# Kernel optimization log

Measured on AMD Instinct MI355X. Metric: run time of the kernel, lower is better.

The kernel has to match this reference:

```python
import jax, jax.numpy as jnp
import numpy as np

N = 5000
NFEAT = 512
NHID = 64
NHEADS = 8
NCLASS = 40
ALPHA = 0.2  # leaky relu slope
NEG_INF = -9e15


def setup_inputs() -> dict:
    key = jax.random.key(0)
    ks = jax.random.split(key, 12)
    x = jax.random.normal(ks[0], (N, NFEAT), dtype=jnp.float32)
    # binary adjacency, ~32 avg degree, with self loops
    adj = (jax.random.uniform(ks[1], (N, N)) < (32.0 / N)).astype(jnp.float32)
    adj = jnp.maximum(adj, jnp.eye(N, dtype=jnp.float32))
    s = 1.0 / np.sqrt(NFEAT)
    W_h = jax.random.uniform(ks[2], (NHEADS, NFEAT, NHID), minval=-s, maxval=s, dtype=jnp.float32)
    a_h = jax.random.uniform(ks[3], (NHEADS, 2 * NHID), minval=-s, maxval=s, dtype=jnp.float32)
    s2 = 1.0 / np.sqrt(NHID * NHEADS)
    W_o = jax.random.uniform(ks[4], (NHID * NHEADS, NHID), minval=-s2, maxval=s2, dtype=jnp.float32)
    a_o = jax.random.uniform(ks[5], (2 * NHID,), minval=-s2, maxval=s2, dtype=jnp.float32)
    s3 = 1.0 / np.sqrt(NHID)
    fc1_w = jax.random.uniform(ks[6], (NHID, 200), minval=-s3, maxval=s3, dtype=jnp.float32)
    fc1_b = jax.random.uniform(ks[7], (200,), minval=-s3, maxval=s3, dtype=jnp.float32)
    s4 = 1.0 / np.sqrt(200)
    fc2_w = jax.random.uniform(ks[8], (200, NCLASS), minval=-s4, maxval=s4, dtype=jnp.float32)
    fc2_b = jax.random.uniform(ks[9], (NCLASS,), minval=-s4, maxval=s4, dtype=jnp.float32)
    return {"x": x, "adj": adj, "W_h": W_h, "a_h": a_h, "W_o": W_o, "a_o": a_o,
            "fc1_w": fc1_w, "fc1_b": fc1_b, "fc2_w": fc2_w, "fc2_b": fc2_b}


def _masked_attention(e, adj):
    # e: [..., N, N]; mask where adj == 0, then row softmax
    e = jnp.where(adj > 0, e, NEG_INF)
    return jax.nn.softmax(e, axis=-1)


def reference(x, adj, W_h, a_h, W_o, a_o, fc1_w, fc1_b, fc2_w, fc2_b):
    # ---- multi-head GAT layer (concat=True), eval mode (dropout off) ----
    Wh = jnp.einsum('nf,hfo->hno', x, W_h)                 # [H, N, nhid]
    f1 = jnp.einsum('hno,ho->hn', Wh, a_h[:, :NHID])       # [H, N]
    f2 = jnp.einsum('hno,ho->hn', Wh, a_h[:, NHID:])       # [H, N]
    e = jax.nn.leaky_relu(f1[:, :, None] + f2[:, None, :], ALPHA)  # [H, N, N]
    att = _masked_attention(e, adj[None, :, :])
    h = jnp.einsum('hnm,hmo->hno', att, Wh)                # [H, N, nhid]
    h1 = jax.nn.elu(h).transpose(1, 0, 2).reshape(N, NHEADS * NHID)  # concat heads

    # ---- output GAT layer (concat=False) ----
    Wh2 = h1 @ W_o                                         # [N, nhid]
    g1 = Wh2 @ a_o[:NHID]                                  # [N]
    g2 = Wh2 @ a_o[NHID:]                                  # [N]
    e2 = jax.nn.leaky_relu(g1[:, None] + g2[None, :], ALPHA)
    att2 = _masked_attention(e2, adj)
    h2 = att2 @ Wh2                                        # [N, nhid]

    # ---- MLP head ----
    h3 = jax.nn.elu(h2 @ fc1_w + fc1_b)
    return h3 @ fc2_w + fc2_b                              # [N, nclass]
```

## Files before the change

### kernel.cpp

```cpp
#include <hip/hip_runtime.h>

typedef unsigned short u16;
typedef unsigned int u32;
typedef unsigned long long u64;
typedef __bf16 bf16_t;
typedef __bf16 bf16x8 __attribute__((ext_vector_type(8)));
typedef float f32x4 __attribute__((ext_vector_type(4)));
typedef u32 u32x4 __attribute__((ext_vector_type(4)));

#define NN 5000
#define NF 512
#define NH 64
#define HEADS 8
#define NCLS 40
#define CAP 128
#define LRELU 0.2f

#define CVT_BIG 320
#define CVT_GRID (CVT_BIG + 8)

__device__ __forceinline__ bool adj_is_bf16(const void* adj) {
    return ((*(const u32*)adj) & 0xFFFFu) != 0u;
}
__device__ __forceinline__ u16 rne_bf16(float f) {
    u32 u = __float_as_uint(f);
    u += 0x7FFFu + ((u >> 16) & 1u);
    return (u16)(u >> 16);
}
__device__ __forceinline__ float up_bf16(u16 h) {
    return __uint_as_float((u32)h << 16);
}
__device__ __forceinline__ u32x4 ntload4(const void* p, int idx) {
    return __builtin_nontemporal_load(((const u32x4*)p) + idx);
}

__global__ __launch_bounds__(256) void cvt(const void* __restrict__ x, const void* __restrict__ W_h,
                                           const void* __restrict__ adj,
                                           const void* a_h, const void* W_o, const void* a_o,
                                           const void* f1w, const void* f1b,
                                           const void* f2w, const void* f2b,
                                           u16* __restrict__ xc, u16* __restrict__ whc,
                                           float* a_hc, float* W_oc, float* a_oc,
                                           float* f1wc, float* f1bc, float* f2wc, float* f2bc) {
    const bool isb = adj_is_bf16(adj);
    const int b = blockIdx.x;
    if (b < CVT_BIG) {
        const int X4 = NN * NF / 4;
        const int T4 = X4 + HEADS * NF * NH / 4;
        for (int i = b * 256 + threadIdx.x; i < T4; i += CVT_BIG * 256) {
            const void* src; u16* dst; int off;
            if (i < X4) { src = x; dst = xc; off = i; }
            else        { src = W_h; dst = whc; off = i - X4; }
            ushort4 o;
            if (isb) {
                o = ((const ushort4*)src)[off];
            } else {
                u32x4 vv = ntload4(src, off);
                o.x = rne_bf16(__uint_as_float(vv[0])); o.y = rne_bf16(__uint_as_float(vv[1]));
                o.z = rne_bf16(__uint_as_float(vv[2])); o.w = rne_bf16(__uint_as_float(vv[3]));
            }
            ((ushort4*)dst)[off] = o;
        }
    } else {
        const int s0 = HEADS * 2 * NH, s1 = HEADS * NH * NH, s2 = 2 * NH,
                  s3 = NH * 200, s4 = 200, s5 = 200 * NCLS, s6 = NCLS;
        const int total = s0 + s1 + s2 + s3 + s4 + s5 + s6;
        for (int i = (b - CVT_BIG) * 256 + threadIdx.x; i < total; i += 8 * 256) {
            const void* src; float* dst; int off = i;
            if (off < s0) { src = a_h; dst = a_hc; }
            else if ((off -= s0) < s1) { src = W_o;  dst = W_oc; }
            else if ((off -= s1) < s2) { src = a_o;  dst = a_oc; }
            else if ((off -= s2) < s3) { src = f1w;  dst = f1wc; }
            else if ((off -= s3) < s4) { src = f1b;  dst = f1bc; }
            else if ((off -= s4) < s5) { src = f2w;  dst = f2wc; }
            else { off -= s5;           src = f2b;  dst = f2bc; }
            dst[off] = isb ? up_bf16(((const u16*)src)[off]) : ((const float*)src)[off];
        }
    }
}

__global__ __launch_bounds__(256) void gemm1_f(const bf16_t* __restrict__ x,
                                               const bf16_t* __restrict__ W_h,
                                               const float* __restrict__ a_h,
                                               float* __restrict__ Wh,
                                               float* __restrict__ f1,
                                               float* __restrict__ f2) {
    const int lane = threadIdx.x & 63;
    const int wid  = threadIdx.x >> 6;
    const int rg = blockIdx.x;
    const int h  = blockIdx.y;
    const int quad = lane >> 4;
    const int lr   = lane & 15;
    const int kq   = quad * 8;
    const int nCol = wid * 16 + lr;
    const bf16_t* Bh = W_h + (size_t)h * NF * NH;
    __shared__ float f1s[4][64], f2s[4][64];

    bf16x8 bfrag[16];
    #pragma unroll
    for (int s = 0; s < 16; ++s) {
        bf16x8 bb;
        #pragma unroll
        for (int j = 0; j < 8; ++j) bb[j] = Bh[(s * 32 + kq + j) * NH + nCol];
        bfrag[s] = bb;
    }
    const float a1c = a_h[h * 128 + nCol];
    const float a2c = a_h[h * 128 + NH + nCol];

    for (int t = 0; t < 4; ++t) {
        const int rb = rg * 64 + t * 16;
        int row  = rb + lr;
        int rowc = row < NN ? row : NN - 1;
        const bf16_t* xp = x + (size_t)rowc * NF + kq;
        f32x4 acc = {0.f, 0.f, 0.f, 0.f};
        #pragma unroll
        for (int s = 0; s < 16; ++s) {
            bf16x8 a = *(const bf16x8*)(xp + s * 32);
            acc = __builtin_amdgcn_mfma_f32_16x16x32_bf16(a, bfrag[s], acc, 0, 0, 0);
        }
        #pragma unroll
        for (int r = 0; r < 4; ++r) {
            int gr = rb + quad * 4 + r;
            if (gr < NN) Wh[(size_t)gr * (HEADS * NH) + h * NH + nCol] = acc[r];
            float p1 = acc[r] * a1c, p2 = acc[r] * a2c;
            #pragma unroll
            for (int o = 8; o; o >>= 1) { p1 += __shfl_xor(p1, o); p2 += __shfl_xor(p2, o); }
            if (lr == 0) { f1s[wid][t * 16 + quad * 4 + r] = p1; f2s[wid][t * 16 + quad * 4 + r] = p2; }
        }
    }
    __syncthreads();
    if (wid == 0) {
        int gr = rg * 64 + lane;
        if (gr < NN) {
            f1[h * NN + gr] = f1s[0][lane] + f1s[1][lane] + f1s[2][lane] + f1s[3][lane];
            f2[h * NN + gr] = f2s[0][lane] + f2s[1][lane] + f2s[2][lane] + f2s[3][lane];
        }
    }
}

__global__ __launch_bounds__(256) void agg1f(const void* __restrict__ adj,
                                             const float* __restrict__ Wh,
                                             const float* __restrict__ f1,
                                             const float* __restrict__ f2,
                                             int* __restrict__ nbr, int* __restrict__ deg,
                                             float* __restrict__ h1) {
    const bool isb = adj_is_bf16(adj);
    const int lane = threadIdx.x & 63;
    const int wid  = threadIdx.x >> 6;
    const int n = blockIdx.x;
    __shared__ int   s_seg[4][CAP];
    __shared__ int   s_cnt[4];
    __shared__ int   s_nbr[CAP];
    const u64 lt = (1ull << lane) - 1;

    int total = 0;
    if (!isb) {
        const float* row = (const float*)adj + (size_t)n * NN;
        const int c0 = wid * 313, cend = min(1250, c0 + 313);
        u32x4 v[5];
        #pragma unroll
        for (int k = 0; k < 5; ++k) {
            int c = c0 + k * 64 + lane;
            v[k] = (c < cend) ? ntload4(row, c) : (u32x4){0u, 0u, 0u, 0u};
        }
        #pragma unroll
        for (int k = 0; k < 5; ++k) {
            int c = c0 + k * 64 + lane;
            #pragma unroll
            for (int j = 0; j < 4; ++j) {
                bool nz = v[k][j] != 0u;
                u64 m = __ballot(nz);
                if (nz) { int pos = total + __popcll(m & lt); if (pos < CAP) s_seg[wid][pos] = c * 4 + j; }
                total += __popcll(m);
            }
        }
    } else {
        const u16* row = (const u16*)adj + (size_t)n * NN;
        const int c0 = wid * 157, cend = min(625, c0 + 157);
        u32x4 v[3];
        #pragma unroll
        for (int k = 0; k < 3; ++k) {
            int c = c0 + k * 64 + lane;
            v[k] = (c < cend) ? ntload4(row, c) : (u32x4){0u, 0u, 0u, 0u};
        }
        #pragma unroll
        for (int k = 0; k < 3; ++k) {
            int c = c0 + k * 64 + lane;
            #pragma unroll
            for (int j = 0; j < 4; ++j) {
                bool nz = (v[k][j] & 0xFFFFu) != 0u;
                u64 m = __ballot(nz);
                if (nz) { int pos = total + __popcll(m & lt); if (pos < CAP) s_seg[wid][pos] = c * 8 + 2 * j; }
                total += __popcll(m);
                bool nz2 = (v[k][j] >> 16) != 0u;
                u64 m2 = __ballot(nz2);
                if (nz2) { int pos = total + __popcll(m2 & lt); if (pos < CAP) s_seg[wid][pos] = c * 8 + 2 * j + 1; }
                total += __popcll(m2);
            }
        }
    }
    if (lane == 0) s_cnt[wid] = total < CAP ? total : CAP;
    __syncthreads();
    const int c0_ = s_cnt[0], c1_ = s_cnt[1], c2_ = s_cnt[2], c3_ = s_cnt[3];
    const int offw = (wid > 0 ? c0_ : 0) + (wid > 1 ? c1_ : 0) + (wid > 2 ? c2_ : 0);
    const int dall0 = c0_ + c1_ + c2_ + c3_;
    const int dall = dall0 < CAP ? dall0 : CAP;
    for (int i = lane; i < s_cnt[wid]; i += 64) {
        int p = offw + i;
        if (p < CAP) s_nbr[p] = s_seg[wid][i];
    }
    __syncthreads();
    for (int i = threadIdx.x; i < dall; i += 256) nbr[(size_t)n * CAP + i] = s_nbr[i];
    if (threadIdx.x == 0) deg[n] = dall;

    const int ha = wid, hb = wid + 4;
    const int nb0 = (lane < dall) ? s_nbr[lane] : 0;
    const int nb1 = (lane + 64 < dall) ? s_nbr[lane + 64] : 0;
    const float f10 = f1[ha * NN + n], f11 = f1[hb * NN + n];
    const float* f2ha = f2 + (size_t)ha * NN;
    const float* f2hb = f2 + (size_t)hb * NN;

    float e00 = -INFINITY, e01 = -INFINITY, e10 = -INFINITY, e11 = -INFINITY;
    if (lane < dall) {
        float a = f10 + f2ha[nb0]; e00 = a > 0.f ? a : LRELU * a;
        float b = f11 + f2hb[nb0]; e10 = b > 0.f ? b : LRELU * b;
    }
    if (lane + 64 < dall) {
        float a = f10 + f2ha[nb1]; e01 = a > 0.f ? a : LRELU * a;
        float b = f11 + f2hb[nb1]; e11 = b > 0.f ? b : LRELU * b;
    }
    float mx0 = fmaxf(e00, e01), mx1 = fmaxf(e10, e11);
    #pragma unroll
    for (int o = 32; o; o >>= 1) {
        mx0 = fmaxf(mx0, __shfl_xor(mx0, o));
        mx1 = fmaxf(mx1, __shfl_xor(mx1, o));
    }
    float p00 = lane < dall ? expf(e00 - mx0) : 0.f;
    float p01 = lane + 64 < dall ? expf(e01 - mx0) : 0.f;
    float p10 = lane < dall ? expf(e10 - mx1) : 0.f;
    float p11 = lane + 64 < dall ? expf(e11 - mx1) : 0.f;
    float sm0 = p00 + p01, sm1 = p10 + p11;
    #pragma unroll
    for (int o = 32; o; o >>= 1) { sm0 += __shfl_xor(sm0, o); sm1 += __shfl_xor(sm1, o); }

    float A0 = 0.f, A1 = 0.f, A2 = 0.f, A3 = 0.f;
    float B0 = 0.f, B1 = 0.f, B2 = 0.f, B3 = 0.f;
    const float* W0 = Wh + ha * NH + lane;
    const float* W1 = Wh + hb * NH + lane;
    int j = 0;
    for (; j + 4 <= dall; j += 4) {
        #pragma unroll
        for (int i = 0; i < 4; ++i) {
            int jj = j + i;
            int sl = jj & 63;
            bool lo = jj < 64;
            int   m  = lo ? __shfl(nb0, sl) : __shfl(nb1, sl);
            float a0 = lo ? __shfl(p00, sl) : __shfl(p01, sl);
            float a1 = lo ? __shfl(p10, sl) : __shfl(p11, sl);
            size_t base = (size_t)m * (HEADS * NH);
            float w0 = W0[base], w1 = W1[base];
            if (i == 0) { A0 += a0 * w0; B0 += a1 * w1; }
            else if (i == 1) { A1 += a0 * w0; B1 += a1 * w1; }
            else if (i == 2) { A2 += a0 * w0; B2 += a1 * w1; }
            else { A3 += a0 * w0; B3 += a1 * w1; }
        }
    }
    for (; j < dall; ++j) {
        int sl = j & 63;
        bool lo = j < 64;
        int   m  = lo ? __shfl(nb0, sl) : __shfl(nb1, sl);
        float a0 = lo ? __shfl(p00, sl) : __shfl(p01, sl);
        float a1 = lo ? __shfl(p10, sl) : __shfl(p11, sl);
        size_t base = (size_t)m * (HEADS * NH);
        A0 += a0 * W0[base]; B0 += a1 * W1[base];
    }
    float hv0 = (A0 + A1 + A2 + A3) / sm0;
    float hv1 = (B0 + B1 + B2 + B3) / sm1;
    hv0 = hv0 > 0.f ? hv0 : expf(hv0) - 1.f;
    hv1 = hv1 > 0.f ? hv1 : expf(hv1) - 1.f;
    h1[(size_t)n * (HEADS * NH) + ha * NH + lane] = hv0;
    h1[(size_t)n * (HEADS * NH) + hb * NH + lane] = hv1;
}

__global__ __launch_bounds__(256) void gemm2_4(const float* __restrict__ h1,
                                               const float* __restrict__ W_o,
                                               const float* __restrict__ a_o,
                                               float* __restrict__ Wh2,
                                               float* __restrict__ g1,
                                               float* __restrict__ g2) {
    const int t = threadIdx.x;
    const int n0 = blockIdx.x * 4;
    __shared__ float sh[4 * 512];
    __shared__ float ps[4][4][64];
    const float4* src = (const float4*)(h1 + (size_t)n0 * 512);
    ((float4*)sh)[t]       = src[t];
    ((float4*)sh)[t + 256] = src[t + 256];
    __syncthreads();
    const int o = t & 63, part = t >> 6;
    float a0 = 0.f, a1 = 0.f, a2 = 0.f, a3 = 0.f;
    const float* wo = W_o + part * 128 * 64 + o;
    const float* s0 = sh + part * 128;
    #pragma unroll 4
    for (int f = 0; f < 128; ++f) {
        float w = wo[f * 64];
        a0 += s0[f] * w; a1 += s0[512 + f] * w; a2 += s0[1024 + f] * w; a3 += s0[1536 + f] * w;
    }
    ps[part][0][o] = a0; ps[part][1][o] = a1; ps[part][2][o] = a2; ps[part][3][o] = a3;
    __syncthreads();
    const int nd = t >> 6;
    float w2 = ps[0][nd][o] + ps[1][nd][o] + ps[2][nd][o] + ps[3][nd][o];
    Wh2[(size_t)(n0 + nd) * 64 + o] = w2;
    float p1 = w2 * a_o[o], p2 = w2 * a_o[64 + o];
    #pragma unroll
    for (int s = 32; s; s >>= 1) { p1 += __shfl_xor(p1, s); p2 += __shfl_xor(p2, s); }
    if (o == 0) { g1[n0 + nd] = p1; g2[n0 + nd] = p2; }
}

__global__ __launch_bounds__(256) void agg2_mlp(const float* __restrict__ Wh2,
                                                const float* __restrict__ g1,
                                                const float* __restrict__ g2,
                                                const int* __restrict__ nbr,
                                                const int* __restrict__ deg,
                                                const float* __restrict__ fc1_w,
                                                const float* __restrict__ fc1_b,
                                                const float* __restrict__ fc2_w,
                                                const float* __restrict__ fc2_b,
                                                float* __restrict__ out) {
    const int lane = threadIdx.x & 63;
    const int wid  = threadIdx.x >> 6;
    const int t = threadIdx.x;
    const int n0 = blockIdx.x * 4;
    const int n = n0 + wid;
    __shared__ float s_alpha[4][CAP];
    __shared__ int   s_nbr[4][CAP];
    __shared__ float s_h2[4][NH];
    __shared__ float s_h3[4][200];
    __shared__ float ps2[2][4][NCLS];
    const int d = deg[n];
    const int* nb = nbr + (size_t)n * CAP;
    const float gn = g1[n];

    float mx = -INFINITY;
    for (int j = lane; j < d; j += 64) {
        int m = nb[j];
        s_nbr[wid][j] = m;
        float e = gn + g2[m];
        e = e > 0.f ? e : LRELU * e;
        s_alpha[wid][j] = e;
        mx = fmaxf(mx, e);
    }
    #pragma unroll
    for (int o = 32; o; o >>= 1) mx = fmaxf(mx, __shfl_xor(mx, o));
    float sm = 0.f;
    for (int j = lane; j < d; j += 64) {
        float p = expf(s_alpha[wid][j] - mx);
        s_alpha[wid][j] = p;
        sm += p;
    }
    #pragma unroll
    for (int o = 32; o; o >>= 1) sm += __shfl_xor(sm, o);

    float acc0 = 0.f, acc1 = 0.f, acc2 = 0.f, acc3 = 0.f;
    int j = 0;
    for (; j + 4 <= d; j += 4) {
        acc0 += s_alpha[wid][j]     * Wh2[(size_t)s_nbr[wid][j]     * NH + lane];
        acc1 += s_alpha[wid][j + 1] * Wh2[(size_t)s_nbr[wid][j + 1] * NH + lane];
        acc2 += s_alpha[wid][j + 2] * Wh2[(size_t)s_nbr[wid][j + 2] * NH + lane];
        acc3 += s_alpha[wid][j + 3] * Wh2[(size_t)s_nbr[wid][j + 3] * NH + lane];
    }
    for (; j < d; ++j) acc0 += s_alpha[wid][j] * Wh2[(size_t)s_nbr[wid][j] * NH + lane];
    s_h2[wid][lane] = (acc0 + acc1 + acc2 + acc3) / sm;
    __syncthreads();

    if (t < 200) {
        float b0 = 0.f, b1 = 0.f, b2 = 0.f, b3 = 0.f;
        #pragma unroll 4
        for (int f = 0; f < NH; ++f) {
            float w = fc1_w[f * 200 + t];
            b0 += s_h2[0][f] * w; b1 += s_h2[1][f] * w; b2 += s_h2[2][f] * w; b3 += s_h2[3][f] * w;
        }
        float bb = fc1_b[t];
        b0 += bb; b1 += bb; b2 += bb; b3 += bb;
        s_h3[0][t] = b0 > 0.f ? b0 : expf(b0) - 1.f;
        s_h3[1][t] = b1 > 0.f ? b1 : expf(b1) - 1.f;
        s_h3[2][t] = b2 > 0.f ? b2 : expf(b2) - 1.f;
        s_h3[3][t] = b3 > 0.f ? b3 : expf(b3) - 1.f;
    }
    __syncthreads();

    if (t < 80) {
        const int o = t % 40, fh = t / 40;
        float c0 = 0.f, c1 = 0.f, c2 = 0.f, c3 = 0.f;
        #pragma unroll 4
        for (int f = fh * 100; f < fh * 100 + 100; ++f) {
            float w = fc2_w[f * NCLS + o];
            c0 += s_h3[0][f] * w; c1 += s_h3[1][f] * w; c2 += s_h3[2][f] * w; c3 += s_h3[3][f] * w;
        }
        ps2[fh][0][o] = c0; ps2[fh][1][o] = c1; ps2[fh][2][o] = c2; ps2[fh][3][o] = c3;
    }
    __syncthreads();
    if (t < 160) {
        const int nd = t / 40, o = t % 40;
        out[(size_t)(n0 + nd) * NCLS + o] = ps2[0][nd][o] + ps2[1][nd][o] + fc2_b[o];
    }
}

extern "C" void kernel_launch(void* const* d_in, const int* in_sizes, int n_in,
                              void* d_out, int out_size, void* d_ws, size_t ws_size,
                              hipStream_t stream) {
    const void* x     = d_in[0];
    const void* adj   = d_in[1];
    const void* W_h   = d_in[2];
    const void* a_h   = d_in[3];
    const void* W_o   = d_in[4];
    const void* a_o   = d_in[5];
    const void* fc1_w = d_in[6];
    const void* fc1_b = d_in[7];
    const void* fc2_w = d_in[8];
    const void* fc2_b = d_in[9];
    float* out = (float*)d_out;

    char* ws = (char*)d_ws;
    int*   nbr   = (int*)(ws + 0);
    int*   deg   = (int*)(ws + 2560000);
    float* Wh    = (float*)(ws + 2580000);
    float* f1    = (float*)(ws + 12820000);
    float* f2    = (float*)(ws + 12980000);
    float* h1    = (float*)(ws + 13140000);
    float* Wh2   = (float*)(ws + 23380000);
    float* g1    = (float*)(ws + 24660000);
    float* g2    = (float*)(ws + 24680000);
    u16*   xc    = (u16*)(ws + 24700000);
    u16*   whc   = (u16*)(ws + 29820000);
    float* a_hc  = (float*)(ws + 30344288);
    float* W_oc  = (float*)(ws + 30348384);
    float* a_oc  = (float*)(ws + 30479456);
    float* f1wc  = (float*)(ws + 30479968);
    float* f1bc  = (float*)(ws + 30531168);
    float* f2wc  = (float*)(ws + 30531968);
    float* f2bc  = (float*)(ws + 30563968);

    cvt<<<CVT_GRID, 256, 0, stream>>>(x, W_h, adj, a_h, W_o, a_o,
                                      fc1_w, fc1_b, fc2_w, fc2_b,
                                      xc, whc, a_hc, W_oc, a_oc,
                                      f1wc, f1bc, f2wc, f2bc);
    gemm1_f<<<dim3(79, HEADS), 256, 0, stream>>>((const bf16_t*)xc, (const bf16_t*)whc,
                                                 a_hc, Wh, f1, f2);
    agg1f<<<NN, 256, 0, stream>>>(adj, Wh, f1, f2, nbr, deg, h1);
    gemm2_4<<<NN / 4, 256, 0, stream>>>(h1, W_oc, a_oc, Wh2, g1, g2);
    agg2_mlp<<<NN / 4, 256, 0, stream>>>(Wh2, g1, g2, nbr, deg,
                                         f1wc, f1bc, f2wc, f2bc, out);
}
```

Measured before the change: 278.3 us.

## Move adjacency scan into conversion kernel as packed bitmask, compact from bitmask

The dense adjacency scan is moved out of the aggregation kernel and into extra blocks of the conversion kernel. Those blocks write a per-row 64-bit ballot bitmask. The aggregation kernel then builds neighbor lists from the 80-word bitmask with one wavefront, using a prefix scan and ffs. The 100MB adjacency read now overlaps with the input conversion instead of sitting on the aggregation critical path. The cost is an extra bitmask buffer, more blocks in the conversion kernel, and serial per-lane bit extraction.

```diff
diff --git a/kernel.cpp b/kernel.cpp
--- a/kernel.cpp
+++ b/kernel.cpp
@@ -15,9 +15,11 @@
 #define NCLS 40
 #define CAP 128
 #define LRELU 0.2f
+#define BMW 80
 
 #define CVT_BIG 320
-#define CVT_GRID (CVT_BIG + 8)
+#define BM_BLKS 1250
+#define CVT_GRID (CVT_BIG + 8 + BM_BLKS)
 
 __device__ __forceinline__ bool adj_is_bf16(const void* adj) {
     return ((*(const u32*)adj) & 0xFFFFu) != 0u;
@@ -41,7 +43,8 @@
                                            const void* f2w, const void* f2b,
                                            u16* __restrict__ xc, u16* __restrict__ whc,
                                            float* a_hc, float* W_oc, float* a_oc,
-                                           float* f1wc, float* f1bc, float* f2wc, float* f2bc) {
+                                           float* f1wc, float* f1bc, float* f2wc, float* f2bc,
+                                           u64* __restrict__ bm) {
     const bool isb = adj_is_bf16(adj);
     const int b = blockIdx.x;
     if (b < CVT_BIG) {
@@ -61,7 +64,7 @@
             }
             ((ushort4*)dst)[off] = o;
         }
-    } else {
+    } else if (b < CVT_BIG + 8) {
         const int s0 = HEADS * 2 * NH, s1 = HEADS * NH * NH, s2 = 2 * NH,
                   s3 = NH * 200, s4 = 200, s5 = 200 * NCLS, s6 = NCLS;
         const int total = s0 + s1 + s2 + s3 + s4 + s5 + s6;
@@ -75,6 +78,50 @@
             else if ((off -= s4) < s5) { src = f2w;  dst = f2wc; }
             else { off -= s5;           src = f2b;  dst = f2bc; }
             dst[off] = isb ? up_bf16(((const u16*)src)[off]) : ((const float*)src)[off];
+        }
+    } else {
+        const int lane = threadIdx.x & 63;
+        const int wid  = threadIdx.x >> 6;
+        const int r = (b - CVT_BIG - 8) * 4 + wid;
+        u64* bmrow = bm + (size_t)r * BMW;
+        if (!isb) {
+            const float* row = (const float*)adj + (size_t)r * NN;
+            #pragma unroll
+            for (int pass = 0; pass < 2; ++pass) {
+                u32x4 v[10];
+                #pragma unroll
+                for (int k = 0; k < 10; ++k) {
+                    int c = (pass * 10 + k) * 64 + lane;
+                    v[k] = (c < 1250) ? ntload4(row, c) : (u32x4){0u, 0u, 0u, 0u};
+                }
+                #pragma unroll
+                for (int k = 0; k < 10; ++k) {
+                    int i = pass * 10 + k;
+                    #pragma unroll
+                    for (int j = 0; j < 4; ++j) {
+                        u64 m = __ballot(v[k][j] != 0u);
+                        if (lane == j) bmrow[i * 4 + j] = m;
+                    }
+                }
+            }
+        } else {
+            const u16* row = (const u16*)adj + (size_t)r * NN;
+            u32x4 v[10];
+            #pragma unroll
+            for (int k = 0; k < 10; ++k) {
+                int c = k * 64 + lane;
+                v[k] = (c < 625) ? ntload4(row, c) : (u32x4){0u, 0u, 0u, 0u};
+            }
+            #pragma unroll
+            for (int k = 0; k < 10; ++k) {
+                #pragma unroll
+                for (int j = 0; j < 4; ++j) {
+                    u64 mlo = __ballot((v[k][j] & 0xFFFFu) != 0u);
+                    u64 mhi = __ballot((v[k][j] >> 16) != 0u);
+                    if (lane == 2 * j)     bmrow[k * 8 + 2 * j]     = mlo;
+                    if (lane == 2 * j + 1) bmrow[k * 8 + 2 * j + 1] = mhi;
+                }
+            }
         }
     }
 }
@@ -139,6 +186,7 @@
 }
 
 __global__ __launch_bounds__(256) void agg1f(const void* __restrict__ adj,
+                                             const u64* __restrict__ bm,
                                              const float* __restrict__ Wh,
                                              const float* __restrict__ f1,
                                              const float* __restrict__ f2,
@@ -148,68 +196,39 @@
     const int lane = threadIdx.x & 63;
     const int wid  = threadIdx.x >> 6;
     const int n = blockIdx.x;
-    __shared__ int   s_seg[4][CAP];
-    __shared__ int   s_cnt[4];
-    __shared__ int   s_nbr[CAP];
-    const u64 lt = (1ull << lane) - 1;
-
-    int total = 0;
-    if (!isb) {
-        const float* row = (const float*)adj + (size_t)n * NN;
-        const int c0 = wid * 313, cend = min(1250, c0 + 313);
-        u32x4 v[5];
+    __shared__ int s_nbr[CAP];
+    __shared__ int s_dall;
+
+    if (wid == 0) {
+        const u64* bmrow = bm + (size_t)n * BMW;
+        int base = 0;
         #pragma unroll
-        for (int k = 0; k < 5; ++k) {
-            int c = c0 + k * 64 + lane;
-            v[k] = (c < cend) ? ntload4(row, c) : (u32x4){0u, 0u, 0u, 0u};
-        }
-        #pragma unroll
-        for (int k = 0; k < 5; ++k) {
-            int c = c0 + k * 64 + lane;
+        for (int r2 = 0; r2 < 2; ++r2) {
+            int w = r2 * 64 + lane;
+            u64 mw = (w < BMW) ? bmrow[w] : 0ull;
+            int pc = __popcll(mw);
+            int scan = pc;
             #pragma unroll
-            for (int j = 0; j < 4; ++j) {
-                bool nz = v[k][j] != 0u;
-                u64 m = __ballot(nz);
-                if (nz) { int pos = total + __popcll(m & lt); if (pos < CAP) s_seg[wid][pos] = c * 4 + j; }
-                total += __popcll(m);
-            }
-        }
-    } else {
-        const u16* row = (const u16*)adj + (size_t)n * NN;
-        const int c0 = wid * 157, cend = min(625, c0 + 157);
-        u32x4 v[3];
-        #pragma unroll
-        for (int k = 0; k < 3; ++k) {
-            int c = c0 + k * 64 + lane;
-            v[k] = (c < cend) ? ntload4(row, c) : (u32x4){0u, 0u, 0u, 0u};
-        }
-        #pragma unroll
-        for (int k = 0; k < 3; ++k) {
-            int c = c0 + k * 64 + lane;
-            #pragma unroll
-            for (int j = 0; j < 4; ++j) {
-                bool nz = (v[k][j] & 0xFFFFu) != 0u;
-                u64 m = __ballot(nz);
-                if (nz) { int pos = total + __popcll(m & lt); if (pos < CAP) s_seg[wid][pos] = c * 8 + 2 * j; }
-                total += __popcll(m);
-                bool nz2 = (v[k][j] >> 16) != 0u;
-                u64 m2 = __ballot(nz2);
-                if (nz2) { int pos = total + __popcll(m2 & lt); if (pos < CAP) s_seg[wid][pos] = c * 8 + 2 * j + 1; }
-                total += __popcll(m2);
-            }
-        }
-    }
-    if (lane == 0) s_cnt[wid] = total < CAP ? total : CAP;
-    __syncthreads();
-    const int c0_ = s_cnt[0], c1_ = s_cnt[1], c2_ = s_cnt[2], c3_ = s_cnt[3];
-    const int offw = (wid > 0 ? c0_ : 0) + (wid > 1 ? c1_ : 0) + (wid > 2 ? c2_ : 0);
-    const int dall0 = c0_ + c1_ + c2_ + c3_;
-    const int dall = dall0 < CAP ? dall0 : CAP;
-    for (int i = lane; i < s_cnt[wid]; i += 64) {
-        int p = offw + i;
-        if (p < CAP) s_nbr[p] = s_seg[wid][i];
-    }
-    __syncthreads();
+            for (int o = 1; o < 64; o <<= 1) {
+                int t = __shfl_up(scan, o);
+                if (lane >= o) scan += t;
+            }
+            int off = base + scan - pc;
+            while (mw) {
+                int bb = __ffsll(mw) - 1;
+                mw &= mw - 1;
+                int elem;
+                if (!isb) elem = ((w >> 2) * 64 + bb) * 4 + (w & 3);
+                else      elem = ((w >> 3) * 64 + bb) * 8 + (w & 7);
+                if (off < CAP) s_nbr[off] = elem;
+                ++off;
+            }
+            base += __shfl(scan, 63);
+        }
+        if (lane == 0) s_dall = base < CAP ? base : CAP;
+    }
+    __syncthreads();
+    const int dall = s_dall;
     for (int i = threadIdx.x; i < dall; i += 256) nbr[(size_t)n * CAP + i] = s_nbr[i];
     if (threadIdx.x == 0) deg[n] = dall;
 
@@ -439,14 +458,15 @@
     float* f1bc  = (float*)(ws + 30531168);
     float* f2wc  = (float*)(ws + 30531968);
     float* f2bc  = (float*)(ws + 30563968);
+    u64*   bm    = (u64*)(ws + 30564128);
 
     cvt<<<CVT_GRID, 256, 0, stream>>>(x, W_h, adj, a_h, W_o, a_o,
                                       fc1_w, fc1_b, fc2_w, fc2_b,
                                       xc, whc, a_hc, W_oc, a_oc,
-                                      f1wc, f1bc, f2wc, f2bc);
+                                      f1wc, f1bc, f2wc, f2bc, bm);
     gemm1_f<<<dim3(79, HEADS), 256, 0, stream>>>((const bf16_t*)xc, (const bf16_t*)whc,
                                                  a_hc, Wh, f1, f2);
-    agg1f<<<NN, 256, 0, stream>>>(adj, Wh, f1, f2, nbr, deg, h1);
+    agg1f<<<NN, 256, 0, stream>>>(adj, bm, Wh, f1, f2, nbr, deg, h1);
     gemm2_4<<<NN / 4, 256, 0, stream>>>(h1, W_oc, a_oc, Wh2, g1, g2);
     agg2_mlp<<<NN / 4, 256, 0, stream>>>(Wh2, g1, g2, nbr, deg,
                                          f1wc, f1bc, f2wc, f2bc, out);
```

Result: no change. 277.6 us (median of 2 runs) (-0.2%).
